# Kernel optimization log

Hardware: AMD Instinct MI355X
Metric: run time of the kernel (lower is better)

The kernel has to match this reference:

```python
import jax, jax.numpy as jnp
import numpy as np

B, T, I, H, L, O = 64, 512, 128, 1024, 4, 128


def setup_inputs() -> dict:
    key = jax.random.key(0)
    ks = jax.random.split(key, 12)
    s_in = 1.0 / np.sqrt(H)  # PyTorch RNN init scale
    inp = {
        "x": jax.random.normal(ks[0], (B, T, I), jnp.float32),
        "hidden": jax.random.normal(ks[1], (L, B, H), jnp.float32) * 0.1,
        # layer 0 weights (input_size -> hidden)
        "W_ih0": jax.random.uniform(ks[2], (H, I), jnp.float32, -s_in, s_in),
        "W_hh0": jax.random.uniform(ks[3], (H, H), jnp.float32, -s_in, s_in),
        "b_ih0": jax.random.uniform(ks[4], (H,), jnp.float32, -s_in, s_in),
        "b_hh0": jax.random.uniform(ks[5], (H,), jnp.float32, -s_in, s_in),
        # layers 1..L-1 (hidden -> hidden), stacked
        "W_ih": jax.random.uniform(ks[6], (L - 1, H, H), jnp.float32, -s_in, s_in),
        "W_hh": jax.random.uniform(ks[7], (L - 1, H, H), jnp.float32, -s_in, s_in),
        "b_ih": jax.random.uniform(ks[8], (L - 1, H), jnp.float32, -s_in, s_in),
        "b_hh": jax.random.uniform(ks[9], (L - 1, H), jnp.float32, -s_in, s_in),
        # output projection
        "W_fc": jax.random.uniform(ks[10], (O, H), jnp.float32, -s_in, s_in),
        "b_fc": jax.random.uniform(ks[11], (O,), jnp.float32, -s_in, s_in),
    }
    return inp


def _run_layer(xs, h0, Wih, Whh, bih, bhh):
    # xs: [B, T, D_in]; h0: [B, H]. PyTorch RNN (relu):
    # h_t = relu(x_t @ Wih^T + b_ih + h_{t-1} @ Whh^T + b_hh)
    # Input projection is time-parallel; only the recurrence is scanned.
    xin = jnp.einsum('btd,hd->bth', xs, Wih) + bih + bhh  # [B,T,H]
    def step(h, x_t):
        h = jax.nn.relu(x_t + h @ Whh.T)
        return h, h
    h_last, ys = jax.lax.scan(step, h0, jnp.swapaxes(xin, 0, 1))  # ys: [T,B,H]
    return jnp.swapaxes(ys, 0, 1), h_last


def reference(x, hidden, W_ih0, W_hh0, b_ih0, b_hh0, W_ih, W_hh, b_ih, b_hh, W_fc, b_fc):
    out, h0_last = _run_layer(x, hidden[0], W_ih0, W_hh0, b_ih0, b_hh0)
    h_lasts = [h0_last]
    for l in range(L - 1):
        out, h_l = _run_layer(out, hidden[l + 1], W_ih[l], W_hh[l], b_ih[l], b_hh[l])
        h_lasts.append(h_l)
    output = jnp.einsum('bth,oh->bto', out, W_fc) + b_fc  # [B,T,O]
    h_n = jnp.stack(h_lasts, axis=0)  # [L,B,H]
    return output, h_n
```

## Files before the change

### kernel.cpp

```cpp
#include <hip/hip_runtime.h>

#define B_ 64
#define T_ 512
#define I_ 128
#define H_ 1024
#define L_ 4
#define O_ 128
#define M_ (B_ * T_)
#define D_ 32

typedef __attribute__((ext_vector_type(8))) short bf16x8_t;
typedef __attribute__((ext_vector_type(4))) float f32x4_t;

__device__ __forceinline__ unsigned short f2bf(float x) {
  unsigned int u = __builtin_bit_cast(unsigned int, x);
  u += 0x7FFFu + ((u >> 16) & 1u);
  return (unsigned short)(u >> 16);
}
__device__ __forceinline__ float bf2f(unsigned short h) {
  return __builtin_bit_cast(float, ((unsigned int)h) << 16);
}
__device__ __forceinline__ f32x4_t mfma16(bf16x8_t a, bf16x8_t b, f32x4_t c) {
  return __builtin_amdgcn_mfma_f32_16x16x32_bf16(a, b, c, 0, 0, 0);
}

__device__ __forceinline__ unsigned aldc(const unsigned* p) {
  return __hip_atomic_load(p, __ATOMIC_RELAXED, __HIP_MEMORY_SCOPE_AGENT);
}
__device__ __forceinline__ unsigned long long ald64(const unsigned long long* p) {
  return __hip_atomic_load(p, __ATOMIC_RELAXED, __HIP_MEMORY_SCOPE_AGENT);
}
__device__ __forceinline__ void ast32(unsigned* p, unsigned v) {
  __hip_atomic_store(p, v, __ATOMIC_RELAXED, __HIP_MEMORY_SCOPE_AGENT);
}

__device__ __forceinline__ unsigned wait_ge(const unsigned* base, unsigned target) {
  const int i = threadIdx.x & 15;
  unsigned v;
  while (true) {
    v = aldc(base + i * 32);
    if (__ballot(v < target) == 0ull) break;
    __builtin_amdgcn_s_sleep(2);
  }
  unsigned mn = v;
  mn = min(mn, (unsigned)__shfl_xor((int)mn, 1));
  mn = min(mn, (unsigned)__shfl_xor((int)mn, 2));
  mn = min(mn, (unsigned)__shfl_xor((int)mn, 4));
  mn = min(mn, (unsigned)__shfl_xor((int)mn, 8));
  return mn;
}

template <int K, int N, bool ASPLIT, bool OUTBF16>
__global__ __launch_bounds__(256, 2) void gemm_k(
    const void* __restrict__ Aq, const float* __restrict__ Wf,
    const float* __restrict__ bias1, const float* __restrict__ bias2,
    void* __restrict__ Cq) {
  extern __shared__ unsigned short smem[];
  unsigned short* Ahi = smem;
  unsigned short* Alo = Ahi + (ASPLIT ? 8192 : 0);
  unsigned short* Bhi = Alo + 8192;
  unsigned short* Blo = Bhi + 8192;

  const int tid = threadIdx.x;
  const int wave = tid >> 6, lane = tid & 63;
  const int wm = wave >> 1, wn = wave & 1;
  const int lm = lane & 15, lk = lane >> 4;
  const int m0 = blockIdx.y * 128, n0 = blockIdx.x * 128;

  f32x4_t acc[4][4] = {};

  for (int kc = 0; kc < K; kc += 64) {
    __syncthreads();
#pragma unroll
    for (int p = 0; p < 4; ++p) {
      int fl = p * 256 + tid;
      int row = fl & 127, ko = (fl >> 7) & 3, kit = fl >> 9;
      int kk = kc + kit * 32 + ko * 8;
      if (ASPLIT) {
        const float* src = (const float*)Aq + (size_t)(m0 + row) * K + kk;
        union { bf16x8_t s; unsigned short u[8]; } th, tl;
#pragma unroll
        for (int e = 0; e < 8; ++e) {
          float v = src[e];
          unsigned short h = f2bf(v);
          th.u[e] = (short)h;
          tl.u[e] = (short)f2bf(v - bf2f(h));
        }
        *(bf16x8_t*)(Ahi + (size_t)fl * 8) = th.s;
        *(bf16x8_t*)(Alo + (size_t)fl * 8) = tl.s;
      } else {
        const unsigned short* src = (const unsigned short*)Aq + (size_t)(m0 + row) * K + kk;
        *(bf16x8_t*)(Ahi + (size_t)fl * 8) = *(const bf16x8_t*)src;
      }
    }
#pragma unroll
    for (int p = 0; p < 4; ++p) {
      int fl = p * 256 + tid;
      int row = fl & 127, ko = (fl >> 7) & 3, kit = fl >> 9;
      int kk = kc + kit * 32 + ko * 8;
      const float* src = Wf + (size_t)(n0 + row) * K + kk;
      union { bf16x8_t s; unsigned short u[8]; } th, tl;
#pragma unroll
      for (int e = 0; e < 8; ++e) {
        float v = src[e];
        unsigned short h = f2bf(v);
        th.u[e] = (short)h;
        tl.u[e] = (short)f2bf(v - bf2f(h));
      }
      *(bf16x8_t*)(Bhi + (size_t)fl * 8) = th.s;
      *(bf16x8_t*)(Blo + (size_t)fl * 8) = tl.s;
    }
    __syncthreads();
#pragma unroll
    for (int kit = 0; kit < 2; ++kit) {
      bf16x8_t bhf[4], blf[4];
#pragma unroll
      for (int n = 0; n < 4; ++n) {
        int br = wn * 64 + n * 16 + lm;
        bhf[n] = *(const bf16x8_t*)(Bhi + ((size_t)(kit * 4 + lk) * 128 + br) * 8);
        blf[n] = *(const bf16x8_t*)(Blo + ((size_t)(kit * 4 + lk) * 128 + br) * 8);
      }
#pragma unroll
      for (int m = 0; m < 4; ++m) {
        int ar = wm * 64 + m * 16 + lm;
        bf16x8_t a = *(const bf16x8_t*)(Ahi + ((size_t)(kit * 4 + lk) * 128 + ar) * 8);
        bf16x8_t al;
        if (ASPLIT) al = *(const bf16x8_t*)(Alo + ((size_t)(kit * 4 + lk) * 128 + ar) * 8);
#pragma unroll
        for (int n = 0; n < 4; ++n) {
          acc[m][n] = mfma16(a, bhf[n], acc[m][n]);
          acc[m][n] = mfma16(a, blf[n], acc[m][n]);
          if (ASPLIT) acc[m][n] = mfma16(al, bhf[n], acc[m][n]);
        }
      }
    }
  }
#pragma unroll
  for (int n = 0; n < 4; ++n) {
    int col = n0 + wn * 64 + n * 16 + lm;
    float bv = bias1[col];
    if (bias2 != nullptr) bv += bias2[col];
#pragma unroll
    for (int m = 0; m < 4; ++m) {
#pragma unroll
      for (int r = 0; r < 4; ++r) {
        int row = m0 + wm * 64 + m * 16 + lk * 4 + r;
        float v = acc[m][n][r] + bv;
        if (OUTBF16)
          ((unsigned short*)Cq)[(size_t)row * N + col] = f2bf(v);
        else
          ((float*)Cq)[(size_t)row * N + col] = v;
      }
    }
  }
}

__global__ __launch_bounds__(256) void splitx_k(const float* __restrict__ x,
                                               unsigned short* __restrict__ xhi,
                                               unsigned short* __restrict__ xlo) {
  int i = (blockIdx.x * 256 + threadIdx.x) * 4;
  float4 v = *(const float4*)(x + i);
  ushort4 h, lo;
  h.x = f2bf(v.x); lo.x = f2bf(v.x - bf2f(h.x));
  h.y = f2bf(v.y); lo.y = f2bf(v.y - bf2f(h.y));
  h.z = f2bf(v.z); lo.z = f2bf(v.z - bf2f(h.z));
  h.w = f2bf(v.w); lo.w = f2bf(v.w - bf2f(h.w));
  *(ushort4*)(xhi + i) = h;
  *(ushort4*)(xlo + i) = lo;
}

__global__ __launch_bounds__(256, 1) void rnn_k(
    const float* __restrict__ hidden,
    const float* __restrict__ Wih0, const float* __restrict__ Whh0,
    const float* __restrict__ bih0, const float* __restrict__ bhh0,
    const float* __restrict__ WihL, const float* __restrict__ WhhL,
    const float* __restrict__ bihL, const float* __restrict__ bhhL,
    const unsigned short* __restrict__ xhi, const unsigned short* __restrict__ xlo,
    unsigned short* __restrict__ ring, unsigned short* __restrict__ seqr,
    unsigned short* __restrict__ s3, float* __restrict__ hn,
    unsigned* __restrict__ prog) {
  extern __shared__ char lds[];
  char* ldsH = lds;
  char* ldsS = lds + 32768;
  const int tid = threadIdx.x;
  const int wave = tid >> 6, lane = tid & 63;
  const int lm = lane & 15, lk = lane >> 4;
  const int bid = blockIdx.x;
  const int l = bid >> 6;
  const int sub = bid & 63;
  const int me = sub >> 2, bg = sub & 3;
  const int g = l * 4 + bg;
  const int j0 = me * 64 + wave * 16;
  const int j = j0 + lm;

  const float* Whh = (l == 0) ? Whh0 : WhhL + (size_t)(l - 1) * H_ * H_;
  bf16x8_t bh[32];
#pragma unroll
  for (int kit = 0; kit < 32; ++kit) {
    const float* src = Whh + (size_t)j * H_ + kit * 32 + lk * 8;
    union { bf16x8_t s; unsigned short u[8]; } th;
#pragma unroll
    for (int e = 0; e < 8; ++e) th.u[e] = (short)f2bf(src[e]);
    bh[kit] = th.s;
  }
  bf16x8_t bw[32];
  bf16x8_t w0h[4], w0l[4];
  if (l > 0) {
    const float* Wih = WihL + (size_t)(l - 1) * H_ * H_;
#pragma unroll
    for (int kit = 0; kit < 32; ++kit) {
      const float* src = Wih + (size_t)j * H_ + kit * 32 + lk * 8;
      union { bf16x8_t s; unsigned short u[8]; } th;
#pragma unroll
      for (int e = 0; e < 8; ++e) th.u[e] = (short)f2bf(src[e]);
      bw[kit] = th.s;
    }
  } else {
#pragma unroll
    for (int kit = 0; kit < 4; ++kit) {
      const float* src = Wih0 + (size_t)j * I_ + kit * 32 + lk * 8;
      union { bf16x8_t s; unsigned short u[8]; } th, tl;
#pragma unroll
      for (int e = 0; e < 8; ++e) {
        float v = src[e];
        unsigned short h = f2bf(v);
        th.u[e] = (short)h;
        tl.u[e] = (short)f2bf(v - bf2f(h));
      }
      w0h[kit] = th.s; w0l[kit] = tl.s;
    }
  }
  float bias = (l == 0) ? (bih0[j] + bhh0[j])
                        : (bihL[(size_t)(l - 1) * H_ + j] + bhhL[(size_t)(l - 1) * H_ + j]);

  {
    unsigned* r1 = (unsigned*)(ring + ((size_t)(l * 2 + 1) * 4 + bg) * 16384);
#pragma unroll
    for (int q = 0; q < 2; ++q) {
      int s = q * 256 + tid;
      int J = s >> 6, b16 = (s >> 2) & 15, h4 = s & 3;
      int jj = me * 64 + J * 8 + h4 * 2;
      const float* hp = hidden + (size_t)l * B_ * H_ + (bg * 16 + b16) * H_ + jj;
      unsigned p0 = f2bf(hp[0]), p1 = f2bf(hp[1]);
      ast32(r1 + me * 512 + s, p0 | (p1 << 16));
    }
  }
  __syncthreads();
  if (tid == 0) ast32(prog + (size_t)(g * 16 + me) * 32, 1u);

  const unsigned* ownB = prog + (size_t)g * 512;
  const unsigned* upB = prog + (size_t)((l - 1) * 4 + bg) * 512;
  const unsigned* dnB = prog + (size_t)((l + 1) * 4 + bg) * 512;
  unsigned upMin = 1, dnMin = 1;

  for (int t = 0; t < T_; ++t) {
    unsigned long long stmp[16];
    if (l > 0) {
      if (upMin < (unsigned)(t + 2)) upMin = wait_ge(upB, (unsigned)(t + 2));
      asm volatile("" ::: "memory");
      const unsigned long long* sp = (const unsigned long long*)(seqr +
          ((size_t)((l - 1) * D_ + (t & (D_ - 1))) * 4 + bg) * 16384);
#pragma unroll
      for (int i = 0; i < 16; ++i) stmp[i] = ald64(sp + i * 256 + tid);
    }
    if (l < 3 && t >= D_) {
      if (dnMin < (unsigned)(t - D_ + 2)) dnMin = wait_ge(dnB, (unsigned)(t - D_ + 2));
    }
    wait_ge(ownB, (unsigned)(t + 1));
    asm volatile("" ::: "memory");
    unsigned long long htmp[16];
    const unsigned long long* hp = (const unsigned long long*)(ring +
        ((size_t)(l * 2 + ((t & 1) ^ 1)) * 4 + bg) * 16384);
#pragma unroll
    for (int i = 0; i < 16; ++i) htmp[i] = ald64(hp + i * 256 + tid);
    {
      unsigned long long* dh = (unsigned long long*)ldsH;
#pragma unroll
      for (int i = 0; i < 16; ++i) dh[i * 256 + tid] = htmp[i];
      if (l > 0) {
        unsigned long long* dsp = (unsigned long long*)ldsS;
#pragma unroll
        for (int i = 0; i < 16; ++i) dsp[i * 256 + tid] = stmp[i];
      }
    }
    __syncthreads();
    f32x4_t a0 = {0.f, 0.f, 0.f, 0.f}, a3 = {0.f, 0.f, 0.f, 0.f};
    if (l > 0) {
#pragma unroll
      for (int kit = 0; kit < 32; ++kit) {
        const int fo = ((kit * 4 + lk) * 16 + lm) * 16;
        bf16x8_t ah = *(const bf16x8_t*)(ldsH + fo);
        bf16x8_t as = *(const bf16x8_t*)(ldsS + fo);
        a0 = mfma16(ah, bh[kit], a0);
        a3 = mfma16(as, bw[kit], a3);
      }
    } else {
#pragma unroll
      for (int kit = 0; kit < 32; ++kit) {
        const int fo = ((kit * 4 + lk) * 16 + lm) * 16;
        bf16x8_t ah = *(const bf16x8_t*)(ldsH + fo);
        a0 = mfma16(ah, bh[kit], a0);
      }
      const int b = bg * 16 + lm;
#pragma unroll
      for (int kit = 0; kit < 4; ++kit) {
        const size_t xo = ((size_t)b * T_ + t) * I_ + kit * 32 + lk * 8;
        bf16x8_t xh = *(const bf16x8_t*)(xhi + xo);
        bf16x8_t xl = *(const bf16x8_t*)(xlo + xo);
        a3 = mfma16(xh, w0h[kit], a3);
        a3 = mfma16(xl, w0h[kit], a3);
        a3 = mfma16(xh, w0l[kit], a3);
      }
    }
    unsigned* rwu = (unsigned*)(ring + ((size_t)(l * 2 + (t & 1)) * 4 + bg) * 16384);
    unsigned* swu = (unsigned*)(seqr + ((size_t)(l * D_ + (t & (D_ - 1))) * 4 + bg) * 16384);
#pragma unroll
    for (int r = 0; r < 4; ++r) {
      const int b15 = lk * 4 + r;
      float v = a0[r] + a3[r] + bias;
      v = fmaxf(v, 0.f);
      unsigned hi = f2bf(v);
      unsigned other = (unsigned)__shfl_xor((int)hi, 1);
      if (!(lm & 1)) {
        const unsigned pk = hi | (other << 16);
        const int p32 = ((j >> 3) * 16 + b15) * 4 + ((j & 7) >> 1);
        ast32(rwu + p32, pk);
        if (l < 3) ast32(swu + p32, pk);
      }
      if (l == 3) s3[((size_t)(bg * 16 + b15) * T_ + t) * H_ + j] = (unsigned short)hi;
      if (t == T_ - 1) hn[(size_t)l * B_ * H_ + (bg * 16 + b15) * H_ + j] = v;
    }
    __syncthreads();
    if (tid == 0) ast32(prog + (size_t)(g * 16 + me) * 32, (unsigned)(t + 2));
  }
}

extern "C" void kernel_launch(void* const* d_in, const int* in_sizes, int n_in,
                              void* d_out, int out_size, void* d_ws, size_t ws_size,
                              hipStream_t stream) {
  const float* x = (const float*)d_in[0];
  const float* hidden = (const float*)d_in[1];
  const float* Wih0 = (const float*)d_in[2];
  const float* Whh0 = (const float*)d_in[3];
  const float* bih0 = (const float*)d_in[4];
  const float* bhh0 = (const float*)d_in[5];
  const float* WihL = (const float*)d_in[6];
  const float* WhhL = (const float*)d_in[7];
  const float* bihL = (const float*)d_in[8];
  const float* bhhL = (const float*)d_in[9];
  const float* Wfc = (const float*)d_in[10];
  const float* bfc = (const float*)d_in[11];
  float* out = (float*)d_out;
  float* hn = out + (size_t)M_ * O_;

  char* ws = (char*)d_ws;
  unsigned* prog = (unsigned*)ws;
  unsigned short* ring = (unsigned short*)(ws + 65536);
  unsigned short* seqr = (unsigned short*)(ws + 65536 + (1u << 20));
  unsigned short* s3 = (unsigned short*)(ws + 65536 + (1u << 20) + (12u << 20));
  unsigned short* xhi = (unsigned short*)(ws + 65536 + (1u << 20) + (12u << 20) + (64u << 20));
  unsigned short* xlo = xhi + (size_t)B_ * T_ * I_;

  hipMemsetAsync(ws, 0, 65536, stream);
  splitx_k<<<(B_ * T_ * I_) / 1024, 256, 0, stream>>>(x, xhi, xlo);

  hipFuncSetAttribute((const void*)rnn_k, hipFuncAttributeMaxDynamicSharedMemorySize,
                      64 * 1024);
  rnn_k<<<256, 256, 64 * 1024, stream>>>(hidden, Wih0, Whh0, bih0, bhh0,
                                         WihL, WhhL, bihL, bhhL, xhi, xlo,
                                         ring, seqr, s3, hn, prog);

  gemm_k<H_, O_, false, false><<<dim3(O_ / 128, M_ / 128), 256, 48 * 1024, stream>>>(
      (const void*)s3, Wfc, bfc, nullptr, (void*)out);
}
```

Before: 2.335 ms.

## Precompute next-step input projection off the recurrence critical path

The input-projection MFMA work for step t+1 (layer-below sequence loads, LDS staging and the W_ih product) now runs right after the progress flag for step t is published. This takes it out of the window between waiting on the own-layer hidden state and producing the next state. The recurrent MFMA chain is split into two interleaved accumulators to shorten the dependency chain. The layer-3 output store now happens after the flag, and the own-group wait drops its unused min-reduction. In exchange there is an extra __syncthreads per step inside precompute, and the LDS staging buffer for the sequence input is reused across iterations.

```diff
diff --git a/kernel.cpp b/kernel.cpp
--- a/kernel.cpp
+++ b/kernel.cpp
@@ -48,6 +48,15 @@
   mn = min(mn, (unsigned)__shfl_xor((int)mn, 4));
   mn = min(mn, (unsigned)__shfl_xor((int)mn, 8));
   return mn;
+}
+
+__device__ __forceinline__ void wait_all(const unsigned* base, unsigned target) {
+  const int i = threadIdx.x & 15;
+  while (true) {
+    unsigned v = aldc(base + i * 32);
+    if (__ballot(v < target) == 0ull) break;
+    __builtin_amdgcn_s_sleep(2);
+  }
 }
 
 template <int K, int N, bool ASPLIT, bool OUTBF16>
@@ -252,21 +261,53 @@
   const unsigned* upB = prog + (size_t)((l - 1) * 4 + bg) * 512;
   const unsigned* dnB = prog + (size_t)((l + 1) * 4 + bg) * 512;
   unsigned upMin = 1, dnMin = 1;
+  f32x4_t a3s = {0.f, 0.f, 0.f, 0.f};
+
+  auto precompute = [&](int tt) {
+    if (l > 0) {
+      if (upMin < (unsigned)(tt + 2)) upMin = wait_ge(upB, (unsigned)(tt + 2));
+      asm volatile("" ::: "memory");
+      unsigned long long stmp[16];
+      const unsigned long long* sp = (const unsigned long long*)(seqr +
+          ((size_t)((l - 1) * D_ + (tt & (D_ - 1))) * 4 + bg) * 16384);
+#pragma unroll
+      for (int i = 0; i < 16; ++i) stmp[i] = ald64(sp + i * 256 + tid);
+      unsigned long long* dsp = (unsigned long long*)ldsS;
+#pragma unroll
+      for (int i = 0; i < 16; ++i) dsp[i * 256 + tid] = stmp[i];
+      __syncthreads();
+      f32x4_t xa = {0.f, 0.f, 0.f, 0.f}, xb = {0.f, 0.f, 0.f, 0.f};
+#pragma unroll
+      for (int kit = 0; kit < 32; ++kit) {
+        const int fo = ((kit * 4 + lk) * 16 + lm) * 16;
+        bf16x8_t as = *(const bf16x8_t*)(ldsS + fo);
+        if (kit & 1) xb = mfma16(as, bw[kit], xb);
+        else         xa = mfma16(as, bw[kit], xa);
+      }
+      a3s = xa + xb;
+    } else {
+      const int b = bg * 16 + lm;
+      f32x4_t xa = {0.f, 0.f, 0.f, 0.f}, xb = {0.f, 0.f, 0.f, 0.f};
+#pragma unroll
+      for (int kit = 0; kit < 4; ++kit) {
+        const size_t xo = ((size_t)b * T_ + tt) * I_ + kit * 32 + lk * 8;
+        bf16x8_t xh = *(const bf16x8_t*)(xhi + xo);
+        bf16x8_t xl = *(const bf16x8_t*)(xlo + xo);
+        xa = mfma16(xh, w0h[kit], xa);
+        xb = mfma16(xl, w0h[kit], xb);
+        xa = mfma16(xh, w0l[kit], xa);
+      }
+      a3s = xa + xb;
+    }
+  };
+
+  precompute(0);
 
   for (int t = 0; t < T_; ++t) {
-    unsigned long long stmp[16];
-    if (l > 0) {
-      if (upMin < (unsigned)(t + 2)) upMin = wait_ge(upB, (unsigned)(t + 2));
-      asm volatile("" ::: "memory");
-      const unsigned long long* sp = (const unsigned long long*)(seqr +
-          ((size_t)((l - 1) * D_ + (t & (D_ - 1))) * 4 + bg) * 16384);
-#pragma unroll
-      for (int i = 0; i < 16; ++i) stmp[i] = ald64(sp + i * 256 + tid);
-    }
     if (l < 3 && t >= D_) {
       if (dnMin < (unsigned)(t - D_ + 2)) dnMin = wait_ge(dnB, (unsigned)(t - D_ + 2));
     }
-    wait_ge(ownB, (unsigned)(t + 1));
+    wait_all(ownB, (unsigned)(t + 1));
     asm volatile("" ::: "memory");
     unsigned long long htmp[16];
     const unsigned long long* hp = (const unsigned long long*)(ring +
@@ -277,49 +318,26 @@
       unsigned long long* dh = (unsigned long long*)ldsH;
 #pragma unroll
       for (int i = 0; i < 16; ++i) dh[i * 256 + tid] = htmp[i];
-      if (l > 0) {
-        unsigned long long* dsp = (unsigned long long*)ldsS;
-#pragma unroll
-        for (int i = 0; i < 16; ++i) dsp[i * 256 + tid] = stmp[i];
-      }
     }
     __syncthreads();
-    f32x4_t a0 = {0.f, 0.f, 0.f, 0.f}, a3 = {0.f, 0.f, 0.f, 0.f};
-    if (l > 0) {
-#pragma unroll
-      for (int kit = 0; kit < 32; ++kit) {
-        const int fo = ((kit * 4 + lk) * 16 + lm) * 16;
-        bf16x8_t ah = *(const bf16x8_t*)(ldsH + fo);
-        bf16x8_t as = *(const bf16x8_t*)(ldsS + fo);
-        a0 = mfma16(ah, bh[kit], a0);
-        a3 = mfma16(as, bw[kit], a3);
-      }
-    } else {
-#pragma unroll
-      for (int kit = 0; kit < 32; ++kit) {
-        const int fo = ((kit * 4 + lk) * 16 + lm) * 16;
-        bf16x8_t ah = *(const bf16x8_t*)(ldsH + fo);
-        a0 = mfma16(ah, bh[kit], a0);
-      }
-      const int b = bg * 16 + lm;
-#pragma unroll
-      for (int kit = 0; kit < 4; ++kit) {
-        const size_t xo = ((size_t)b * T_ + t) * I_ + kit * 32 + lk * 8;
-        bf16x8_t xh = *(const bf16x8_t*)(xhi + xo);
-        bf16x8_t xl = *(const bf16x8_t*)(xlo + xo);
-        a3 = mfma16(xh, w0h[kit], a3);
-        a3 = mfma16(xl, w0h[kit], a3);
-        a3 = mfma16(xh, w0l[kit], a3);
-      }
+    f32x4_t h0a = {0.f, 0.f, 0.f, 0.f}, h0b = {0.f, 0.f, 0.f, 0.f};
+#pragma unroll
+    for (int kit = 0; kit < 32; ++kit) {
+      const int fo = ((kit * 4 + lk) * 16 + lm) * 16;
+      bf16x8_t ah = *(const bf16x8_t*)(ldsH + fo);
+      if (kit & 1) h0b = mfma16(ah, bh[kit], h0b);
+      else         h0a = mfma16(ah, bh[kit], h0a);
     }
     unsigned* rwu = (unsigned*)(ring + ((size_t)(l * 2 + (t & 1)) * 4 + bg) * 16384);
     unsigned* swu = (unsigned*)(seqr + ((size_t)(l * D_ + (t & (D_ - 1))) * 4 + bg) * 16384);
+    unsigned hi4[4];
 #pragma unroll
     for (int r = 0; r < 4; ++r) {
       const int b15 = lk * 4 + r;
-      float v = a0[r] + a3[r] + bias;
+      float v = h0a[r] + h0b[r] + a3s[r] + bias;
       v = fmaxf(v, 0.f);
       unsigned hi = f2bf(v);
+      hi4[r] = hi;
       unsigned other = (unsigned)__shfl_xor((int)hi, 1);
       if (!(lm & 1)) {
         const unsigned pk = hi | (other << 16);
@@ -327,11 +345,16 @@
         ast32(rwu + p32, pk);
         if (l < 3) ast32(swu + p32, pk);
       }
-      if (l == 3) s3[((size_t)(bg * 16 + b15) * T_ + t) * H_ + j] = (unsigned short)hi;
       if (t == T_ - 1) hn[(size_t)l * B_ * H_ + (bg * 16 + b15) * H_ + j] = v;
     }
     __syncthreads();
     if (tid == 0) ast32(prog + (size_t)(g * 16 + me) * 32, (unsigned)(t + 2));
+    if (l == 3) {
+#pragma unroll
+      for (int r = 0; r < 4; ++r)
+        s3[((size_t)(bg * 16 + lk * 4 + r) * T_ + t) * H_ + j] = (unsigned short)hi4[r];
+    }
+    if (t + 1 < T_) precompute(t + 1);
   }
 }
 
```

After: 1.950 ms. -16.5%, faster.
